# Optimization experiments

Hardware: AMD Instinct MI355X
Metric: run time of the kernel (lower is better)

Reference implementation:

```python
import jax, jax.numpy as jnp
import numpy as np

B, L, C, H = 4, 1024, 768, 12
D = C // H  # head_ch = 64


def setup_inputs() -> dict:
    key = jax.random.key(0)
    ks = jax.random.split(key, 8)
    s = 1.0 / np.sqrt(C)
    return {
        "inputs_q": jax.random.normal(ks[0], (B, L, C), jnp.float32),
        "inputs_kv": jax.random.normal(ks[1], (B, L, C), jnp.float32),
        "Wq": jax.random.normal(ks[2], (C, H * D), jnp.float32) * s,
        "Wk": jax.random.normal(ks[3], (C, H * D), jnp.float32) * s,
        "Wv": jax.random.normal(ks[4], (C, H * D), jnp.float32) * s,
        "Wout": jax.random.normal(ks[5], (H * D, C), jnp.float32) * s,
        "W_pre": jax.random.normal(ks[6], (H, H), jnp.float32) * (1.0 / np.sqrt(H)),
        "W_post": jax.random.normal(ks[7], (H, H), jnp.float32) * (1.0 / np.sqrt(H)),
    }


def reference(inputs_q, inputs_kv, Wq, Wk, Wv, Wout, W_pre, W_post):
    # Linear projections (no bias), split into heads: b l (h d) -> b h l d
    def split_heads(x):
        b, l, _ = x.shape
        return x.reshape(b, l, H, D).transpose(0, 2, 1, 3)

    q = split_heads(inputs_q @ Wq) / jnp.sqrt(jnp.asarray(D, inputs_q.dtype))
    k = split_heads(inputs_kv @ Wk)
    v = split_heads(inputs_kv @ Wv)

    # Attention logits [b, h, l, k]
    weights = jnp.einsum('bhld,bhkd->bhlk', q, k)
    # Talking-heads: learned cross-head mixing pre-softmax
    weights = jnp.einsum('bhlk,hi->bilk', weights, W_pre)
    weights = jax.nn.softmax(weights, axis=-1)
    # Talking-heads post-softmax mixing
    weights = jnp.einsum('bhlk,hi->bilk', weights, W_post)

    scores = jnp.einsum('bhlk,bhkd->bhld', weights, v)
    scores = scores.transpose(0, 2, 1, 3).reshape(B, L, H * D)  # b l (h d)
    return scores @ Wout
```

## Files before the change

kernel.cpp:

```cpp
#include <hip/hip_runtime.h>

#define BB 4
#define LL 1024
#define CC 768
#define HH 12
#define DD 64

typedef unsigned short ushort_t;
typedef __attribute__((ext_vector_type(8))) short bf16x8;
typedef __attribute__((ext_vector_type(4))) float f32x4;
typedef __attribute__((ext_vector_type(2))) float f32x2;

__device__ inline ushort_t f2bf(float x) {
    union { float f; unsigned u; } v; v.f = x;
    unsigned r = (v.u + 0x7FFFu + ((v.u >> 16) & 1u)) >> 16;
    return (ushort_t)r;
}
__device__ inline float bf2f(ushort_t u) {
    union { unsigned u; float f; } v; v.u = ((unsigned)u) << 16;
    return v.f;
}
__device__ inline float u2f(unsigned u) {
    union { unsigned u; float f; } v; v.u = u;
    return v.f;
}

__device__ inline void stage_rows(const ushort_t* __restrict__ g, int stride,
                                  ushort_t* lds, int nbytes, int wave, int lane) {
    const int ko = (lane & 3) << 3;
    const int rsub = lane >> 2;
    for (int off = wave * 1024; off < nbytes; off += 4096) {
        int row = (off >> 6) + rsub;
        __builtin_amdgcn_global_load_lds(
            (const __attribute__((address_space(1))) void*)(g + (size_t)row * stride + ko),
            (__attribute__((address_space(3))) void*)(lds + (off >> 1)),
            16, 0, 0);
    }
}

__global__ __launch_bounds__(256) void prep(const float* __restrict__ q, const float* __restrict__ kv,
                                            const float* __restrict__ w0, const float* __restrict__ w1,
                                            const float* __restrict__ w2, const float* __restrict__ w3,
                                            ushort_t* __restrict__ qo, ushort_t* __restrict__ kvo,
                                            ushort_t* __restrict__ o0, ushort_t* __restrict__ o1,
                                            ushort_t* __restrict__ o2, ushort_t* __restrict__ o3) {
    __shared__ float t[32][33];
    const int bx = blockIdx.x;
    if (bx < 3072) {
        const float* src = bx < 1536 ? q : kv;
        ushort_t* dst = bx < 1536 ? qo : kvo;
        int bb = bx < 1536 ? bx : bx - 1536;
        size_t i = ((size_t)bb * 256 + threadIdx.x) * 8;
        float4 a = *(const float4*)(src + i);
        float4 b = *(const float4*)(src + i + 4);
        ushort_t u[8] = {f2bf(a.x), f2bf(a.y), f2bf(a.z), f2bf(a.w),
                         f2bf(b.x), f2bf(b.y), f2bf(b.z), f2bf(b.w)};
        *(uint4*)(dst + i) = *(uint4*)u;
    } else {
        int w = bx - 3072;
        int z = w / 576, rem = w % 576;
        const float* W = z == 0 ? w0 : z == 1 ? w1 : z == 2 ? w2 : w3;
        ushort_t* Wt   = z == 0 ? o0 : z == 1 ? o1 : z == 2 ? o2 : o3;
        const int c = threadIdx.x & 31, r0 = threadIdx.x >> 5;
        const int kb = (rem / 24) * 32, nb = (rem % 24) * 32;
#pragma unroll
        for (int i = 0; i < 4; ++i)
            t[r0 + 8 * i][c] = W[(size_t)(kb + r0 + 8 * i) * CC + nb + c];
        __syncthreads();
#pragma unroll
        for (int i = 0; i < 4; ++i)
            Wt[(size_t)(nb + r0 + 8 * i) * CC + kb + c] = f2bf(t[c][r0 + 8 * i]);
    }
}

__global__ __launch_bounds__(256) void proj_gemm(const ushort_t* __restrict__ Aq,
                                                 const ushort_t* __restrict__ Akv,
                                                 const ushort_t* __restrict__ Wqt,
                                                 const ushort_t* __restrict__ Wkt,
                                                 const ushort_t* __restrict__ Wvt,
                                                 ushort_t* __restrict__ Qo,
                                                 ushort_t* __restrict__ Ko,
                                                 ushort_t* __restrict__ Vto) {
    const int z = blockIdx.z;
    const ushort_t* A  = (z == 0) ? Aq : Akv;
    const ushort_t* Wt = (z == 0) ? Wqt : (z == 1 ? Wkt : Wvt);

    __shared__ __align__(16) ushort_t a_lds[128 * 32];
    __shared__ __align__(16) ushort_t b_lds[128 * 32];

    const int tid = threadIdx.x;
    const int bm = blockIdx.x * 128, bn = blockIdx.y * 128;
    const int wave = tid >> 6, lane = tid & 63;
    const int quad = lane >> 4, lq = lane & 15;
    const int wr = wave >> 1, wc = wave & 1;

    f32x4 acc[4][4] = {};

    for (int k0 = 0; k0 < CC; k0 += 32) {
        stage_rows(A + (size_t)bm * CC + k0, CC, a_lds, 8192, wave, lane);
        stage_rows(Wt + (size_t)bn * CC + k0, CC, b_lds, 8192, wave, lane);
        __syncthreads();
        bf16x8 af[4], bfr[4];
#pragma unroll
        for (int mi = 0; mi < 4; ++mi)
            af[mi] = *(bf16x8*)&a_lds[(wr * 64 + mi * 16 + lq) * 32 + quad * 8];
#pragma unroll
        for (int ni = 0; ni < 4; ++ni)
            bfr[ni] = *(bf16x8*)&b_lds[(wc * 64 + ni * 16 + lq) * 32 + quad * 8];
#pragma unroll
        for (int mi = 0; mi < 4; ++mi)
#pragma unroll
            for (int ni = 0; ni < 4; ++ni)
                acc[mi][ni] = __builtin_amdgcn_mfma_f32_16x16x32_bf16(af[mi], bfr[ni], acc[mi][ni], 0, 0, 0);
        __syncthreads();
    }

    const float scale = (z == 0) ? 0.125f : 1.0f;
#pragma unroll
    for (int mi = 0; mi < 4; ++mi)
#pragma unroll
        for (int ni = 0; ni < 4; ++ni)
#pragma unroll
            for (int r = 0; r < 4; ++r) {
                int row = bm + wr * 64 + mi * 16 + quad * 4 + r;
                int col = bn + wc * 64 + ni * 16 + lq;
                int b = row >> 10, l = row & 1023, h = col >> 6, d = col & 63;
                ushort_t v = f2bf(acc[mi][ni][r] * scale);
                if (z == 0)      Qo[((size_t)(b * HH + h) * LL + l) * DD + d] = v;
                else if (z == 1) Ko[((size_t)(b * HH + h) * LL + l) * DD + d] = v;
                else             Vto[((size_t)(b * HH + h) * DD + d) * LL + l] = v;
            }
}

__global__ __launch_bounds__(256) void qk_gemm(const ushort_t* __restrict__ Q,
                                               const ushort_t* __restrict__ K,
                                               ushort_t* __restrict__ S) {
    __shared__ __align__(16) ushort_t a_lds[128 * 32];
    __shared__ __align__(16) ushort_t b_lds[128 * 32];

    const int tid = threadIdx.x;
    const int bm = blockIdx.x * 128, bn = blockIdx.y * 128;
    const int bh = blockIdx.z;
    const ushort_t* Qh = Q + (size_t)bh * LL * DD;
    const ushort_t* Kh = K + (size_t)bh * LL * DD;
    const int wave = tid >> 6, lane = tid & 63;
    const int quad = lane >> 4, lq = lane & 15;
    const int wr = wave >> 1, wc = wave & 1;

    f32x4 acc[4][4] = {};

    for (int k0 = 0; k0 < DD; k0 += 32) {
        stage_rows(Qh + (size_t)bm * DD + k0, DD, a_lds, 8192, wave, lane);
        stage_rows(Kh + (size_t)bn * DD + k0, DD, b_lds, 8192, wave, lane);
        __syncthreads();
        bf16x8 af[4], bfr[4];
#pragma unroll
        for (int mi = 0; mi < 4; ++mi)
            af[mi] = *(bf16x8*)&a_lds[(wr * 64 + mi * 16 + lq) * 32 + quad * 8];
#pragma unroll
        for (int ni = 0; ni < 4; ++ni)
            bfr[ni] = *(bf16x8*)&b_lds[(wc * 64 + ni * 16 + lq) * 32 + quad * 8];
#pragma unroll
        for (int mi = 0; mi < 4; ++mi)
#pragma unroll
            for (int ni = 0; ni < 4; ++ni)
                acc[mi][ni] = __builtin_amdgcn_mfma_f32_16x16x32_bf16(af[mi], bfr[ni], acc[mi][ni], 0, 0, 0);
        __syncthreads();
    }

#pragma unroll
    for (int mi = 0; mi < 4; ++mi)
#pragma unroll
        for (int ni = 0; ni < 4; ++ni)
#pragma unroll
            for (int r = 0; r < 4; ++r) {
                int row = bm + wr * 64 + mi * 16 + quad * 4 + r;
                int col = bn + wc * 64 + ni * 16 + lq;
                S[((size_t)bh * LL + row) * LL + col] = f2bf(acc[mi][ni][r]);
            }
}

__global__ __launch_bounds__(256) void mix_softmax(ushort_t* __restrict__ S,
                                                   const float* __restrict__ Wpre,
                                                   const float* __restrict__ Wpost) {
    __shared__ float reds[4][16];

    const int tid = threadIdx.x;
    const int wave = tid >> 6, lane = tid & 63;
    const int l = blockIdx.x, b = blockIdx.y;

    const size_t hstride = (size_t)LL * LL;
    const size_t base = ((size_t)(b * HH) * LL + l) * LL + tid * 4;

    f32x2 p[HH][2];
#pragma unroll
    for (int i = 0; i < HH; ++i) { p[i][0] = 0.f; p[i][1] = 0.f; }
#pragma unroll
    for (int h = 0; h < HH; ++h) {
        uint2 raw = *(const uint2*)&S[base + h * hstride];
        f32x2 v0, v1;
        v0.x = u2f(raw.x << 16); v0.y = u2f(raw.x & 0xFFFF0000u);
        v1.x = u2f(raw.y << 16); v1.y = u2f(raw.y & 0xFFFF0000u);
#pragma unroll
        for (int i = 0; i < HH; ++i) {
            float w = Wpre[h * HH + i];
            p[i][0] += v0 * w;
            p[i][1] += v1 * w;
        }
    }

    float sm[HH];
#pragma unroll
    for (int i = 0; i < HH; ++i) {
        p[i][0].x = __expf(p[i][0].x); p[i][0].y = __expf(p[i][0].y);
        p[i][1].x = __expf(p[i][1].x); p[i][1].y = __expf(p[i][1].y);
        f32x2 t2 = p[i][0] + p[i][1];
        float ss = t2.x + t2.y;
#pragma unroll
        for (int off = 32; off; off >>= 1) ss += __shfl_xor(ss, off);
        sm[i] = ss;
    }
    if (lane == 0) {
#pragma unroll
        for (int i = 0; i < HH; ++i) reds[wave][i] = sm[i];
    }
    __syncthreads();
#pragma unroll
    for (int i = 0; i < HH; ++i) {
        float tot = (reds[0][i] + reds[1][i]) + (reds[2][i] + reds[3][i]);
        float inv = 1.0f / tot;
        p[i][0] *= inv; p[i][1] *= inv;
    }

#pragma unroll
    for (int i = 0; i < HH; ++i) {
        f32x2 a0 = 0.f, a1 = 0.f;
#pragma unroll
        for (int h = 0; h < HH; ++h) {
            float w = Wpost[h * HH + i];
            a0 += p[h][0] * w;
            a1 += p[h][1] * w;
        }
        ushort_t u[4] = {f2bf(a0.x), f2bf(a0.y), f2bf(a1.x), f2bf(a1.y)};
        *(uint2*)&S[base + i * hstride] = *(uint2*)u;
    }
}

__global__ __launch_bounds__(256) void pv_gemm(const ushort_t* __restrict__ P,
                                               const ushort_t* __restrict__ Vt,
                                               ushort_t* __restrict__ att) {
    __shared__ __align__(16) ushort_t a_lds[64 * 32];
    __shared__ __align__(16) ushort_t b_lds[64 * 32];

    const int tid = threadIdx.x;
    const int bm = blockIdx.x * 64;
    const int bh = blockIdx.y;
    const int b = bh / HH, ih = bh % HH;
    const ushort_t* Ph = P + ((size_t)bh << 20);
    const ushort_t* Vh = Vt + (size_t)bh * LL * DD;
    const int wave = tid >> 6, lane = tid & 63;
    const int quad = lane >> 4, lq = lane & 15;
    const int wr = wave >> 1, wc = wave & 1;

    f32x4 acc[2][2] = {};

    for (int k0 = 0; k0 < LL; k0 += 32) {
        stage_rows(Ph + (size_t)bm * LL + k0, LL, a_lds, 4096, wave, lane);
        stage_rows(Vh + k0, LL, b_lds, 4096, wave, lane);
        __syncthreads();
        bf16x8 af[2], bfr[2];
#pragma unroll
        for (int mi = 0; mi < 2; ++mi)
            af[mi] = *(bf16x8*)&a_lds[(wr * 32 + mi * 16 + lq) * 32 + quad * 8];
#pragma unroll
        for (int ni = 0; ni < 2; ++ni)
            bfr[ni] = *(bf16x8*)&b_lds[(wc * 32 + ni * 16 + lq) * 32 + quad * 8];
#pragma unroll
        for (int mi = 0; mi < 2; ++mi)
#pragma unroll
            for (int ni = 0; ni < 2; ++ni)
                acc[mi][ni] = __builtin_amdgcn_mfma_f32_16x16x32_bf16(af[mi], bfr[ni], acc[mi][ni], 0, 0, 0);
        __syncthreads();
    }

#pragma unroll
    for (int mi = 0; mi < 2; ++mi)
#pragma unroll
        for (int ni = 0; ni < 2; ++ni)
#pragma unroll
            for (int r = 0; r < 4; ++r) {
                int lrow = bm + wr * 32 + mi * 16 + quad * 4 + r;
                int col = wc * 32 + ni * 16 + lq;
                att[((size_t)(b * LL) + lrow) * CC + ih * DD + col] = f2bf(acc[mi][ni][r]);
            }
}

__global__ __launch_bounds__(256) void out_gemm(const ushort_t* __restrict__ A,
                                                const ushort_t* __restrict__ Wt,
                                                float* __restrict__ out) {
    __shared__ __align__(16) ushort_t a_lds[128 * 32];
    __shared__ __align__(16) ushort_t b_lds[64 * 32];

    const int tid = threadIdx.x;
    const int bm = blockIdx.x * 128, bn = blockIdx.y * 64;
    const int wave = tid >> 6, lane = tid & 63;
    const int quad = lane >> 4, lq = lane & 15;
    const int wr = wave >> 1, wc = wave & 1;

    f32x4 acc[4][2] = {};

    for (int k0 = 0; k0 < CC; k0 += 32) {
        stage_rows(A + (size_t)bm * CC + k0, CC, a_lds, 8192, wave, lane);
        stage_rows(Wt + (size_t)bn * CC + k0, CC, b_lds, 4096, wave, lane);
        __syncthreads();
        bf16x8 af[4], bfr[2];
#pragma unroll
        for (int mi = 0; mi < 4; ++mi)
            af[mi] = *(bf16x8*)&a_lds[(wr * 64 + mi * 16 + lq) * 32 + quad * 8];
#pragma unroll
        for (int ni = 0; ni < 2; ++ni)
            bfr[ni] = *(bf16x8*)&b_lds[(wc * 32 + ni * 16 + lq) * 32 + quad * 8];
#pragma unroll
        for (int mi = 0; mi < 4; ++mi)
#pragma unroll
            for (int ni = 0; ni < 2; ++ni)
                acc[mi][ni] = __builtin_amdgcn_mfma_f32_16x16x32_bf16(af[mi], bfr[ni], acc[mi][ni], 0, 0, 0);
        __syncthreads();
    }

#pragma unroll
    for (int mi = 0; mi < 4; ++mi)
#pragma unroll
        for (int ni = 0; ni < 2; ++ni)
#pragma unroll
            for (int r = 0; r < 4; ++r) {
                int row = bm + wr * 64 + mi * 16 + quad * 4 + r;
                int col = bn + wc * 32 + ni * 16 + lq;
                out[(size_t)row * CC + col] = acc[mi][ni][r];
            }
}

extern "C" void kernel_launch(void* const* d_in, const int* in_sizes, int n_in,
                              void* d_out, int out_size, void* d_ws, size_t ws_size,
                              hipStream_t stream) {
    const float* inputs_q  = (const float*)d_in[0];
    const float* inputs_kv = (const float*)d_in[1];
    const float* Wq   = (const float*)d_in[2];
    const float* Wk   = (const float*)d_in[3];
    const float* Wv   = (const float*)d_in[4];
    const float* Wout = (const float*)d_in[5];
    const float* Wpre  = (const float*)d_in[6];
    const float* Wpost = (const float*)d_in[7];
    float* out = (float*)d_out;

    const size_t nS   = (size_t)BB * HH * LL * LL;
    const size_t nQKV = (size_t)BB * HH * LL * DD;
    const size_t nW   = (size_t)CC * CC;

    ushort_t* Sb   = (ushort_t*)d_ws;
    ushort_t* Qb   = Sb + nS;
    ushort_t* Kb   = Qb + nQKV;
    ushort_t* Vtb  = Kb + nQKV;
    ushort_t* attb = Vtb + nQKV;
    ushort_t* inq  = attb + nQKV;
    ushort_t* inkv = inq + nQKV;
    ushort_t* Wqt  = inkv + nQKV;
    ushort_t* Wkt  = Wqt + nW;
    ushort_t* Wvt  = Wkt + nW;
    ushort_t* Wot  = Wvt + nW;

    dim3 blk(256);

    prep<<<dim3(5376), blk, 0, stream>>>(inputs_q, inputs_kv, Wq, Wk, Wv, Wout,
                                         inq, inkv, Wqt, Wkt, Wvt, Wot);
    proj_gemm<<<dim3(32, 6, 3), blk, 0, stream>>>(inq, inkv, Wqt, Wkt, Wvt, Qb, Kb, Vtb);
    qk_gemm<<<dim3(8, 8, BB * HH), blk, 0, stream>>>(Qb, Kb, Sb);
    mix_softmax<<<dim3(LL, BB), blk, 0, stream>>>(Sb, Wpre, Wpost);
    pv_gemm<<<dim3(16, BB * HH), blk, 0, stream>>>(Sb, Vtb, attb);
    out_gemm<<<dim3(32, 12), blk, 0, stream>>>(attb, Wot, out);
}
```

Measured before the change: 232.6 us.

## Fuse pre-mix into QK GEMM and softmax/post-mix into PV GEMM

```diff
diff --git a/kernel.cpp b/kernel.cpp
--- a/kernel.cpp
+++ b/kernel.cpp
@@ -132,167 +132,197 @@
             }
 }
 
-__global__ __launch_bounds__(256) void qk_gemm(const ushort_t* __restrict__ Q,
-                                               const ushort_t* __restrict__ K,
-                                               ushort_t* __restrict__ S) {
-    __shared__ __align__(16) ushort_t a_lds[128 * 32];
-    __shared__ __align__(16) ushort_t b_lds[128 * 32];
+__global__ __launch_bounds__(256) void qk_premix(const ushort_t* __restrict__ Q,
+                                                 const ushort_t* __restrict__ K,
+                                                 const float* __restrict__ Wpre,
+                                                 ushort_t* __restrict__ S,
+                                                 float* __restrict__ z) {
+    __shared__ __align__(16) ushort_t qt[2][128 * 32];
+    __shared__ __align__(16) ushort_t kt[2][64 * 32];
+    __shared__ __align__(16) ushort_t T[HH * 64 * 32];
 
     const int tid = threadIdx.x;
-    const int bm = blockIdx.x * 128, bn = blockIdx.y * 128;
-    const int bh = blockIdx.z;
-    const ushort_t* Qh = Q + (size_t)bh * LL * DD;
-    const ushort_t* Kh = K + (size_t)bh * LL * DD;
+    const int k0 = blockIdx.x * 32, l0 = blockIdx.y * 64, b = blockIdx.z;
     const int wave = tid >> 6, lane = tid & 63;
     const int quad = lane >> 4, lq = lane & 15;
-    const int wr = wave >> 1, wc = wave & 1;
-
-    f32x4 acc[4][4] = {};
-
-    for (int k0 = 0; k0 < DD; k0 += 32) {
-        stage_rows(Qh + (size_t)bm * DD + k0, DD, a_lds, 8192, wave, lane);
-        stage_rows(Kh + (size_t)bn * DD + k0, DD, b_lds, 8192, wave, lane);
-        __syncthreads();
-        bf16x8 af[4], bfr[4];
-#pragma unroll
-        for (int mi = 0; mi < 4; ++mi)
-            af[mi] = *(bf16x8*)&a_lds[(wr * 64 + mi * 16 + lq) * 32 + quad * 8];
-#pragma unroll
-        for (int ni = 0; ni < 4; ++ni)
-            bfr[ni] = *(bf16x8*)&b_lds[(wc * 64 + ni * 16 + lq) * 32 + quad * 8];
-#pragma unroll
-        for (int mi = 0; mi < 4; ++mi)
-#pragma unroll
-            for (int ni = 0; ni < 4; ++ni)
-                acc[mi][ni] = __builtin_amdgcn_mfma_f32_16x16x32_bf16(af[mi], bfr[ni], acc[mi][ni], 0, 0, 0);
-        __syncthreads();
-    }
-
-#pragma unroll
-    for (int mi = 0; mi < 4; ++mi)
-#pragma unroll
-        for (int ni = 0; ni < 4; ++ni)
+
+    {
+        const ushort_t* Qh = Q + ((size_t)(b * HH) * LL + l0) * DD;
+        const ushort_t* Kh = K + ((size_t)(b * HH) * LL + k0) * DD;
+        stage_rows(Qh,      DD, qt[0],        4096, wave, lane);
+        stage_rows(Qh + 32, DD, qt[0] + 2048, 4096, wave, lane);
+        stage_rows(Kh,      DD, kt[0],        2048, wave, lane);
+        stage_rows(Kh + 32, DD, kt[0] + 1024, 2048, wave, lane);
+    }
+
+    for (int h = 0; h < HH; ++h) {
+        const int cur = h & 1, nxt = cur ^ 1;
+        __syncthreads();
+        if (h + 1 < HH) {
+            const ushort_t* Qh = Q + ((size_t)(b * HH + h + 1) * LL + l0) * DD;
+            const ushort_t* Kh = K + ((size_t)(b * HH + h + 1) * LL + k0) * DD;
+            stage_rows(Qh,      DD, qt[nxt],        4096, wave, lane);
+            stage_rows(Qh + 32, DD, qt[nxt] + 2048, 4096, wave, lane);
+            stage_rows(Kh,      DD, kt[nxt],        2048, wave, lane);
+            stage_rows(Kh + 32, DD, kt[nxt] + 1024, 2048, wave, lane);
+        }
+        f32x4 acc[2] = {};
+#pragma unroll
+        for (int ks = 0; ks < 2; ++ks) {
+            bf16x8 af = *(bf16x8*)&qt[cur][(ks * 64 + wave * 16 + lq) * 32 + quad * 8];
+#pragma unroll
+            for (int nt = 0; nt < 2; ++nt) {
+                bf16x8 bf = *(bf16x8*)&kt[cur][(ks * 32 + nt * 16 + lq) * 32 + quad * 8];
+                acc[nt] = __builtin_amdgcn_mfma_f32_16x16x32_bf16(af, bf, acc[nt], 0, 0, 0);
+            }
+        }
+#pragma unroll
+        for (int nt = 0; nt < 2; ++nt)
 #pragma unroll
             for (int r = 0; r < 4; ++r) {
-                int row = bm + wr * 64 + mi * 16 + quad * 4 + r;
-                int col = bn + wc * 64 + ni * 16 + lq;
-                S[((size_t)bh * LL + row) * LL + col] = f2bf(acc[mi][ni][r]);
-            }
-}
-
-__global__ __launch_bounds__(256) void mix_softmax(ushort_t* __restrict__ S,
-                                                   const float* __restrict__ Wpre,
-                                                   const float* __restrict__ Wpost) {
-    __shared__ float reds[4][16];
-
-    const int tid = threadIdx.x;
-    const int wave = tid >> 6, lane = tid & 63;
-    const int l = blockIdx.x, b = blockIdx.y;
-
-    const size_t hstride = (size_t)LL * LL;
-    const size_t base = ((size_t)(b * HH) * LL + l) * LL + tid * 4;
-
-    f32x2 p[HH][2];
-#pragma unroll
-    for (int i = 0; i < HH; ++i) { p[i][0] = 0.f; p[i][1] = 0.f; }
+                int l = wave * 16 + quad * 4 + r;
+                T[(h * 64 + l) * 32 + nt * 16 + lq] = f2bf(acc[nt][r]);
+            }
+    }
+    __syncthreads();
+
+    const int l = tid >> 2, k8 = (tid & 3) * 8;
+    f32x2 pa[HH][4];
+#pragma unroll
+    for (int i = 0; i < HH; ++i) { pa[i][0] = 0.f; pa[i][1] = 0.f; pa[i][2] = 0.f; pa[i][3] = 0.f; }
 #pragma unroll
     for (int h = 0; h < HH; ++h) {
-        uint2 raw = *(const uint2*)&S[base + h * hstride];
-        f32x2 v0, v1;
-        v0.x = u2f(raw.x << 16); v0.y = u2f(raw.x & 0xFFFF0000u);
-        v1.x = u2f(raw.y << 16); v1.y = u2f(raw.y & 0xFFFF0000u);
+        uint4 raw = *(uint4*)&T[(h * 64 + l) * 32 + k8];
+        f32x2 v[4];
+        v[0].x = u2f(raw.x << 16); v[0].y = u2f(raw.x & 0xFFFF0000u);
+        v[1].x = u2f(raw.y << 16); v[1].y = u2f(raw.y & 0xFFFF0000u);
+        v[2].x = u2f(raw.z << 16); v[2].y = u2f(raw.z & 0xFFFF0000u);
+        v[3].x = u2f(raw.w << 16); v[3].y = u2f(raw.w & 0xFFFF0000u);
 #pragma unroll
         for (int i = 0; i < HH; ++i) {
             float w = Wpre[h * HH + i];
-            p[i][0] += v0 * w;
-            p[i][1] += v1 * w;
-        }
-    }
-
-    float sm[HH];
+            pa[i][0] += v[0] * w; pa[i][1] += v[1] * w;
+            pa[i][2] += v[2] * w; pa[i][3] += v[3] * w;
+        }
+    }
+
+    float zs[HH];
 #pragma unroll
     for (int i = 0; i < HH; ++i) {
-        p[i][0].x = __expf(p[i][0].x); p[i][0].y = __expf(p[i][0].y);
-        p[i][1].x = __expf(p[i][1].x); p[i][1].y = __expf(p[i][1].y);
-        f32x2 t2 = p[i][0] + p[i][1];
-        float ss = t2.x + t2.y;
-#pragma unroll
-        for (int off = 32; off; off >>= 1) ss += __shfl_xor(ss, off);
-        sm[i] = ss;
-    }
-    if (lane == 0) {
-#pragma unroll
-        for (int i = 0; i < HH; ++i) reds[wave][i] = sm[i];
-    }
-    __syncthreads();
+        ushort_t u[8];
+        float e = 0.f;
+#pragma unroll
+        for (int j = 0; j < 4; ++j) {
+            u[2 * j]     = f2bf(pa[i][j].x);
+            u[2 * j + 1] = f2bf(pa[i][j].y);
+            e += __expf(bf2f(u[2 * j])) + __expf(bf2f(u[2 * j + 1]));
+        }
+        zs[i] = e;
+        *(uint4*)&S[((size_t)(b * HH + i) * LL + l0 + l) * LL + k0 + k8] = *(uint4*)u;
+    }
 #pragma unroll
     for (int i = 0; i < HH; ++i) {
-        float tot = (reds[0][i] + reds[1][i]) + (reds[2][i] + reds[3][i]);
-        float inv = 1.0f / tot;
-        p[i][0] *= inv; p[i][1] *= inv;
-    }
-
-#pragma unroll
-    for (int i = 0; i < HH; ++i) {
-        f32x2 a0 = 0.f, a1 = 0.f;
-#pragma unroll
-        for (int h = 0; h < HH; ++h) {
-            float w = Wpost[h * HH + i];
-            a0 += p[h][0] * w;
-            a1 += p[h][1] * w;
-        }
-        ushort_t u[4] = {f2bf(a0.x), f2bf(a0.y), f2bf(a1.x), f2bf(a1.y)};
-        *(uint2*)&S[base + i * hstride] = *(uint2*)u;
-    }
-}
-
-__global__ __launch_bounds__(256) void pv_gemm(const ushort_t* __restrict__ P,
-                                               const ushort_t* __restrict__ Vt,
-                                               ushort_t* __restrict__ att) {
-    __shared__ __align__(16) ushort_t a_lds[64 * 32];
-    __shared__ __align__(16) ushort_t b_lds[64 * 32];
+        float zr = zs[i];
+        zr += __shfl_xor(zr, 1);
+        zr += __shfl_xor(zr, 2);
+        if ((tid & 3) == 0)
+            atomicAdd(&z[(size_t)(b * HH + i) * LL + l0 + l], zr);
+    }
+}
+
+__global__ __launch_bounds__(256) void pv_fused(const ushort_t* __restrict__ S,
+                                                const ushort_t* __restrict__ Vt,
+                                                const float* __restrict__ z,
+                                                const float* __restrict__ Wpost,
+                                                ushort_t* __restrict__ att) {
+    __shared__ __align__(16) ushort_t sp[2][HH * 16 * 32];
+    __shared__ __align__(16) ushort_t vt[2][HH * 64 * 32];
+    __shared__ __align__(16) ushort_t pp[HH * 16 * 40];
 
     const int tid = threadIdx.x;
-    const int bm = blockIdx.x * 64;
-    const int bh = blockIdx.y;
-    const int b = bh / HH, ih = bh % HH;
-    const ushort_t* Ph = P + ((size_t)bh << 20);
-    const ushort_t* Vh = Vt + (size_t)bh * LL * DD;
+    const int l0 = blockIdx.x * 16, b = blockIdx.y;
     const int wave = tid >> 6, lane = tid & 63;
     const int quad = lane >> 4, lq = lane & 15;
-    const int wr = wave >> 1, wc = wave & 1;
-
-    f32x4 acc[2][2] = {};
-
-    for (int k0 = 0; k0 < LL; k0 += 32) {
-        stage_rows(Ph + (size_t)bm * LL + k0, LL, a_lds, 4096, wave, lane);
-        stage_rows(Vh + k0, LL, b_lds, 4096, wave, lane);
-        __syncthreads();
-        bf16x8 af[2], bfr[2];
-#pragma unroll
-        for (int mi = 0; mi < 2; ++mi)
-            af[mi] = *(bf16x8*)&a_lds[(wr * 32 + mi * 16 + lq) * 32 + quad * 8];
-#pragma unroll
-        for (int ni = 0; ni < 2; ++ni)
-            bfr[ni] = *(bf16x8*)&b_lds[(wc * 32 + ni * 16 + lq) * 32 + quad * 8];
-#pragma unroll
-        for (int mi = 0; mi < 2; ++mi)
-#pragma unroll
-            for (int ni = 0; ni < 2; ++ni)
-                acc[mi][ni] = __builtin_amdgcn_mfma_f32_16x16x32_bf16(af[mi], bfr[ni], acc[mi][ni], 0, 0, 0);
-        __syncthreads();
-    }
-
-#pragma unroll
-    for (int mi = 0; mi < 2; ++mi)
-#pragma unroll
-        for (int ni = 0; ni < 2; ++ni)
-#pragma unroll
-            for (int r = 0; r < 4; ++r) {
-                int lrow = bm + wr * 32 + mi * 16 + quad * 4 + r;
-                int col = wc * 32 + ni * 16 + lq;
-                att[((size_t)(b * LL) + lrow) * CC + ih * DD + col] = f2bf(acc[mi][ni][r]);
-            }
+    const int co = (tid & 3) * 8, r0 = tid >> 2;
+    const int la = tid >> 4, k2 = (tid & 15) * 2;
+
+    float invr[HH];
+#pragma unroll
+    for (int h = 0; h < HH; ++h)
+        invr[h] = 1.0f / z[(size_t)(b * HH + h) * LL + l0 + la];
+
+#pragma unroll
+    for (int s = 0; s < 3; ++s) {
+        int row = r0 + 64 * s, i = row >> 4, l = row & 15;
+        __builtin_amdgcn_global_load_lds(
+            (const __attribute__((address_space(1))) void*)(S + ((size_t)(b * HH + i) * LL + l0 + l) * LL + co),
+            (__attribute__((address_space(3))) void*)(sp[0] + row * 32 + co), 16, 0, 0);
+    }
+#pragma unroll
+    for (int s = 0; s < 12; ++s) {
+        int row = r0 + 64 * s, i = row >> 6, d = row & 63;
+        __builtin_amdgcn_global_load_lds(
+            (const __attribute__((address_space(1))) void*)(Vt + ((size_t)(b * HH + i) * DD + d) * LL + co),
+            (__attribute__((address_space(3))) void*)(vt[0] + row * 32 + co), 16, 0, 0);
+    }
+
+    f32x4 acco[HH] = {};
+
+    for (int n = 0; n < 32; ++n) {
+        const int cur = n & 1, nxt = cur ^ 1;
+        __syncthreads();
+
+        f32x2 pacc[HH];
+#pragma unroll
+        for (int i = 0; i < HH; ++i) pacc[i] = 0.f;
+#pragma unroll
+        for (int h = 0; h < HH; ++h) {
+            unsigned raw = *(unsigned*)&sp[cur][h * 512 + la * 32 + k2];
+            f32x2 e;
+            e.x = __expf(u2f(raw << 16)) * invr[h];
+            e.y = __expf(u2f(raw & 0xFFFF0000u)) * invr[h];
+#pragma unroll
+            for (int i = 0; i < HH; ++i)
+                pacc[i] += e * Wpost[h * HH + i];
+        }
+#pragma unroll
+        for (int i = 0; i < HH; ++i) {
+            ushort_t u[2] = {f2bf(pacc[i].x), f2bf(pacc[i].y)};
+            *(unsigned*)&pp[i * 640 + la * 40 + k2] = *(unsigned*)u;
+        }
+        __syncthreads();
+
+        if (n + 1 < 32) {
+            int k0n = (n + 1) * 32;
+#pragma unroll
+            for (int s = 0; s < 3; ++s) {
+                int row = r0 + 64 * s, i = row >> 4, l = row & 15;
+                __builtin_amdgcn_global_load_lds(
+                    (const __attribute__((address_space(1))) void*)(S + ((size_t)(b * HH + i) * LL + l0 + l) * LL + k0n + co),
+                    (__attribute__((address_space(3))) void*)(sp[nxt] + row * 32 + co), 16, 0, 0);
+            }
+#pragma unroll
+            for (int s = 0; s < 12; ++s) {
+                int row = r0 + 64 * s, i = row >> 6, d = row & 63;
+                __builtin_amdgcn_global_load_lds(
+                    (const __attribute__((address_space(1))) void*)(Vt + ((size_t)(b * HH + i) * DD + d) * LL + k0n + co),
+                    (__attribute__((address_space(3))) void*)(vt[nxt] + row * 32 + co), 16, 0, 0);
+            }
+        }
+
+#pragma unroll
+        for (int i = 0; i < HH; ++i) {
+            bf16x8 a  = *(bf16x8*)&pp[i * 640 + lq * 40 + quad * 8];
+            bf16x8 bv = *(bf16x8*)&vt[cur][i * 2048 + (wave * 16 + lq) * 32 + quad * 8];
+            acco[i] = __builtin_amdgcn_mfma_f32_16x16x32_bf16(a, bv, acco[i], 0, 0, 0);
+        }
+    }
+
+#pragma unroll
+    for (int i = 0; i < HH; ++i)
+#pragma unroll
+        for (int r = 0; r < 4; ++r)
+            att[((size_t)(b * LL) + l0 + quad * 4 + r) * CC + i * DD + wave * 16 + lq] = f2bf(acco[i][r]);
 }
 
 __global__ __launch_bounds__(256) void out_gemm(const ushort_t* __restrict__ A,
@@ -368,14 +398,15 @@
     ushort_t* Wkt  = Wqt + nW;
     ushort_t* Wvt  = Wkt + nW;
     ushort_t* Wot  = Wvt + nW;
+    float*    zbuf = (float*)(Wot + nW);
 
     dim3 blk(256);
 
+    hipMemsetAsync(zbuf, 0, (size_t)BB * HH * LL * sizeof(float), stream);
     prep<<<dim3(5376), blk, 0, stream>>>(inputs_q, inputs_kv, Wq, Wk, Wv, Wout,
                                          inq, inkv, Wqt, Wkt, Wvt, Wot);
     proj_gemm<<<dim3(32, 6, 3), blk, 0, stream>>>(inq, inkv, Wqt, Wkt, Wvt, Qb, Kb, Vtb);
-    qk_gemm<<<dim3(8, 8, BB * HH), blk, 0, stream>>>(Qb, Kb, Sb);
-    mix_softmax<<<dim3(LL, BB), blk, 0, stream>>>(Sb, Wpre, Wpost);
-    pv_gemm<<<dim3(16, BB * HH), blk, 0, stream>>>(Sb, Vtb, attb);
+    qk_premix<<<dim3(32, 16, BB), blk, 0, stream>>>(Qb, Kb, Wpre, Sb, zbuf);
+    pv_fused<<<dim3(64, BB), blk, 0, stream>>>(Sb, Vtb, zbuf, Wpost, attb);
     out_gemm<<<dim3(32, 12), blk, 0, stream>>>(attb, Wot, out);
 }
```

Measured after the change: 284.9 us. 22.5% more time.

## Fuse pre-softmax head mixing into QK GEMM and streamline post-mix softmax

Applied to the files above, without the earlier changes.

```diff
diff --git a/kernel.cpp b/kernel.cpp
--- a/kernel.cpp
+++ b/kernel.cpp
@@ -132,117 +132,145 @@
             }
 }
 
-__global__ __launch_bounds__(256) void qk_gemm(const ushort_t* __restrict__ Q,
-                                               const ushort_t* __restrict__ K,
-                                               ushort_t* __restrict__ S) {
-    __shared__ __align__(16) ushort_t a_lds[128 * 32];
-    __shared__ __align__(16) ushort_t b_lds[128 * 32];
+__global__ __launch_bounds__(256) void qk_premix(const ushort_t* __restrict__ Q,
+                                                 const ushort_t* __restrict__ K,
+                                                 const float* __restrict__ Wpre,
+                                                 ushort_t* __restrict__ S) {
+    __shared__ __align__(16) ushort_t qt[2][128 * 32];
+    __shared__ __align__(16) ushort_t kt[2][64 * 32];
+    __shared__ __align__(16) ushort_t T[HH * 64 * 32];
 
     const int tid = threadIdx.x;
-    const int bm = blockIdx.x * 128, bn = blockIdx.y * 128;
-    const int bh = blockIdx.z;
-    const ushort_t* Qh = Q + (size_t)bh * LL * DD;
-    const ushort_t* Kh = K + (size_t)bh * LL * DD;
+    const int k0 = blockIdx.x * 32, l0 = blockIdx.y * 64, b = blockIdx.z;
     const int wave = tid >> 6, lane = tid & 63;
     const int quad = lane >> 4, lq = lane & 15;
-    const int wr = wave >> 1, wc = wave & 1;
-
-    f32x4 acc[4][4] = {};
-
-    for (int k0 = 0; k0 < DD; k0 += 32) {
-        stage_rows(Qh + (size_t)bm * DD + k0, DD, a_lds, 8192, wave, lane);
-        stage_rows(Kh + (size_t)bn * DD + k0, DD, b_lds, 8192, wave, lane);
-        __syncthreads();
-        bf16x8 af[4], bfr[4];
-#pragma unroll
-        for (int mi = 0; mi < 4; ++mi)
-            af[mi] = *(bf16x8*)&a_lds[(wr * 64 + mi * 16 + lq) * 32 + quad * 8];
-#pragma unroll
-        for (int ni = 0; ni < 4; ++ni)
-            bfr[ni] = *(bf16x8*)&b_lds[(wc * 64 + ni * 16 + lq) * 32 + quad * 8];
-#pragma unroll
-        for (int mi = 0; mi < 4; ++mi)
-#pragma unroll
-            for (int ni = 0; ni < 4; ++ni)
-                acc[mi][ni] = __builtin_amdgcn_mfma_f32_16x16x32_bf16(af[mi], bfr[ni], acc[mi][ni], 0, 0, 0);
-        __syncthreads();
-    }
-
-#pragma unroll
-    for (int mi = 0; mi < 4; ++mi)
-#pragma unroll
-        for (int ni = 0; ni < 4; ++ni)
+
+    {
+        const ushort_t* Qh = Q + ((size_t)(b * HH) * LL + l0) * DD;
+        const ushort_t* Kh = K + ((size_t)(b * HH) * LL + k0) * DD;
+        stage_rows(Qh,      DD, qt[0],        4096, wave, lane);
+        stage_rows(Qh + 32, DD, qt[0] + 2048, 4096, wave, lane);
+        stage_rows(Kh,      DD, kt[0],        2048, wave, lane);
+        stage_rows(Kh + 32, DD, kt[0] + 1024, 2048, wave, lane);
+    }
+
+    for (int h = 0; h < HH; ++h) {
+        const int cur = h & 1, nxt = cur ^ 1;
+        __syncthreads();
+        if (h + 1 < HH) {
+            const ushort_t* Qh = Q + ((size_t)(b * HH + h + 1) * LL + l0) * DD;
+            const ushort_t* Kh = K + ((size_t)(b * HH + h + 1) * LL + k0) * DD;
+            stage_rows(Qh,      DD, qt[nxt],        4096, wave, lane);
+            stage_rows(Qh + 32, DD, qt[nxt] + 2048, 4096, wave, lane);
+            stage_rows(Kh,      DD, kt[nxt],        2048, wave, lane);
+            stage_rows(Kh + 32, DD, kt[nxt] + 1024, 2048, wave, lane);
+        }
+        f32x4 acc[2] = {};
+#pragma unroll
+        for (int ks = 0; ks < 2; ++ks) {
+            bf16x8 af = *(bf16x8*)&qt[cur][(ks * 64 + wave * 16 + lq) * 32 + quad * 8];
+#pragma unroll
+            for (int nt = 0; nt < 2; ++nt) {
+                bf16x8 bf = *(bf16x8*)&kt[cur][(ks * 32 + nt * 16 + lq) * 32 + quad * 8];
+                acc[nt] = __builtin_amdgcn_mfma_f32_16x16x32_bf16(af, bf, acc[nt], 0, 0, 0);
+            }
+        }
+#pragma unroll
+        for (int nt = 0; nt < 2; ++nt)
 #pragma unroll
             for (int r = 0; r < 4; ++r) {
-                int row = bm + wr * 64 + mi * 16 + quad * 4 + r;
-                int col = bn + wc * 64 + ni * 16 + lq;
-                S[((size_t)bh * LL + row) * LL + col] = f2bf(acc[mi][ni][r]);
+                int l = wave * 16 + quad * 4 + r;
+                T[(h * 64 + l) * 32 + nt * 16 + lq] = f2bf(acc[nt][r]);
             }
-}
-
-__global__ __launch_bounds__(256) void mix_softmax(ushort_t* __restrict__ S,
-                                                   const float* __restrict__ Wpre,
-                                                   const float* __restrict__ Wpost) {
-    __shared__ float reds[4][16];
+    }
+    __syncthreads();
+
+    const int l = tid >> 2, k8 = (tid & 3) * 8;
+    f32x2 pa[HH][4];
+#pragma unroll
+    for (int i = 0; i < HH; ++i) { pa[i][0] = 0.f; pa[i][1] = 0.f; pa[i][2] = 0.f; pa[i][3] = 0.f; }
+#pragma unroll
+    for (int h = 0; h < HH; ++h) {
+        uint4 raw = *(uint4*)&T[(h * 64 + l) * 32 + k8];
+        f32x2 v[4];
+        v[0].x = u2f(raw.x << 16); v[0].y = u2f(raw.x & 0xFFFF0000u);
+        v[1].x = u2f(raw.y << 16); v[1].y = u2f(raw.y & 0xFFFF0000u);
+        v[2].x = u2f(raw.z << 16); v[2].y = u2f(raw.z & 0xFFFF0000u);
+        v[3].x = u2f(raw.w << 16); v[3].y = u2f(raw.w & 0xFFFF0000u);
+#pragma unroll
+        for (int i = 0; i < HH; ++i) {
+            float w = Wpre[h * HH + i];
+            pa[i][0] += v[0] * w; pa[i][1] += v[1] * w;
+            pa[i][2] += v[2] * w; pa[i][3] += v[3] * w;
+        }
+    }
+
+#pragma unroll
+    for (int i = 0; i < HH; ++i) {
+        ushort_t u[8];
+#pragma unroll
+        for (int j = 0; j < 4; ++j) {
+            u[2 * j]     = f2bf(pa[i][j].x);
+            u[2 * j + 1] = f2bf(pa[i][j].y);
+        }
+        *(uint4*)&S[((size_t)(b * HH + i) * LL + l0 + l) * LL + k0 + k8] = *(uint4*)u;
+    }
+}
+
+__global__ __launch_bounds__(256) void post_mix(ushort_t* __restrict__ S,
+                                                const float* __restrict__ Wpost) {
+    __shared__ float red[4][HH];
 
     const int tid = threadIdx.x;
     const int wave = tid >> 6, lane = tid & 63;
-    const int l = blockIdx.x, b = blockIdx.y;
+    const int half = tid >> 7;
+    const int t = tid & 127;
+    const int l = blockIdx.x * 2 + half;
+    const int b = blockIdx.y;
 
     const size_t hstride = (size_t)LL * LL;
-    const size_t base = ((size_t)(b * HH) * LL + l) * LL + tid * 4;
-
-    f32x2 p[HH][2];
-#pragma unroll
-    for (int i = 0; i < HH; ++i) { p[i][0] = 0.f; p[i][1] = 0.f; }
+    const size_t base = ((size_t)(b * HH) * LL + l) * LL + t * 8;
+
+    f32x2 p[HH][4];
+    float sm[HH];
 #pragma unroll
     for (int h = 0; h < HH; ++h) {
-        uint2 raw = *(const uint2*)&S[base + h * hstride];
-        f32x2 v0, v1;
-        v0.x = u2f(raw.x << 16); v0.y = u2f(raw.x & 0xFFFF0000u);
-        v1.x = u2f(raw.y << 16); v1.y = u2f(raw.y & 0xFFFF0000u);
-#pragma unroll
-        for (int i = 0; i < HH; ++i) {
-            float w = Wpre[h * HH + i];
-            p[i][0] += v0 * w;
-            p[i][1] += v1 * w;
-        }
-    }
-
-    float sm[HH];
+        uint4 raw = *(const uint4*)&S[base + h * hstride];
+        p[h][0].x = __expf(u2f(raw.x << 16)); p[h][0].y = __expf(u2f(raw.x & 0xFFFF0000u));
+        p[h][1].x = __expf(u2f(raw.y << 16)); p[h][1].y = __expf(u2f(raw.y & 0xFFFF0000u));
+        p[h][2].x = __expf(u2f(raw.z << 16)); p[h][2].y = __expf(u2f(raw.z & 0xFFFF0000u));
+        p[h][3].x = __expf(u2f(raw.w << 16)); p[h][3].y = __expf(u2f(raw.w & 0xFFFF0000u));
+        f32x2 t2 = (p[h][0] + p[h][1]) + (p[h][2] + p[h][3]);
+        float ss = t2.x + t2.y;
+#pragma unroll
+        for (int off = 32; off; off >>= 1) ss += __shfl_xor(ss, off);
+        sm[h] = ss;
+    }
+    if (lane == 0) {
+#pragma unroll
+        for (int h = 0; h < HH; ++h) red[wave][h] = sm[h];
+    }
+    __syncthreads();
+
+#pragma unroll
+    for (int h = 0; h < HH; ++h) {
+        float tot = red[half * 2][h] + red[half * 2 + 1][h];
+        float inv = 1.0f / tot;
+        p[h][0] *= inv; p[h][1] *= inv; p[h][2] *= inv; p[h][3] *= inv;
+    }
+
 #pragma unroll
     for (int i = 0; i < HH; ++i) {
-        p[i][0].x = __expf(p[i][0].x); p[i][0].y = __expf(p[i][0].y);
-        p[i][1].x = __expf(p[i][1].x); p[i][1].y = __expf(p[i][1].y);
-        f32x2 t2 = p[i][0] + p[i][1];
-        float ss = t2.x + t2.y;
-#pragma unroll
-        for (int off = 32; off; off >>= 1) ss += __shfl_xor(ss, off);
-        sm[i] = ss;
-    }
-    if (lane == 0) {
-#pragma unroll
-        for (int i = 0; i < HH; ++i) reds[wave][i] = sm[i];
-    }
-    __syncthreads();
-#pragma unroll
-    for (int i = 0; i < HH; ++i) {
-        float tot = (reds[0][i] + reds[1][i]) + (reds[2][i] + reds[3][i]);
-        float inv = 1.0f / tot;
-        p[i][0] *= inv; p[i][1] *= inv;
-    }
-
-#pragma unroll
-    for (int i = 0; i < HH; ++i) {
-        f32x2 a0 = 0.f, a1 = 0.f;
+        f32x2 a0 = 0.f, a1 = 0.f, a2 = 0.f, a3 = 0.f;
 #pragma unroll
         for (int h = 0; h < HH; ++h) {
             float w = Wpost[h * HH + i];
-            a0 += p[h][0] * w;
-            a1 += p[h][1] * w;
+            a0 += p[h][0] * w; a1 += p[h][1] * w;
+            a2 += p[h][2] * w; a3 += p[h][3] * w;
         }
-        ushort_t u[4] = {f2bf(a0.x), f2bf(a0.y), f2bf(a1.x), f2bf(a1.y)};
-        *(uint2*)&S[base + i * hstride] = *(uint2*)u;
+        ushort_t u[8] = {f2bf(a0.x), f2bf(a0.y), f2bf(a1.x), f2bf(a1.y),
+                         f2bf(a2.x), f2bf(a2.y), f2bf(a3.x), f2bf(a3.y)};
+        *(uint4*)&S[base + i * hstride] = *(uint4*)u;
     }
 }
 
@@ -374,8 +402,8 @@
     prep<<<dim3(5376), blk, 0, stream>>>(inputs_q, inputs_kv, Wq, Wk, Wv, Wout,
                                          inq, inkv, Wqt, Wkt, Wvt, Wot);
     proj_gemm<<<dim3(32, 6, 3), blk, 0, stream>>>(inq, inkv, Wqt, Wkt, Wvt, Qb, Kb, Vtb);
-    qk_gemm<<<dim3(8, 8, BB * HH), blk, 0, stream>>>(Qb, Kb, Sb);
-    mix_softmax<<<dim3(LL, BB), blk, 0, stream>>>(Sb, Wpre, Wpost);
+    qk_premix<<<dim3(32, 16, BB), blk, 0, stream>>>(Qb, Kb, Wpre, Sb);
+    post_mix<<<dim3(512, BB), blk, 0, stream>>>(Sb, Wpost);
     pv_gemm<<<dim3(16, BB * HH), blk, 0, stream>>>(Sb, Vtb, attb);
     out_gemm<<<dim3(32, 12), blk, 0, stream>>>(attb, Wot, out);
 }
```

After: 255.9 us. 1.1x slower.
